# Kernel tuning notes

Hardware: AMD Instinct MI355X
Metric: run time of the kernel (lower is better)

The kernel has to match this reference:

```python
import jax, jax.numpy as jnp
import numpy as np

I, H, FC = 118, 1024, 16

def gru_cell(x, h, Wih, Whh, bih, bhh):
    # torch GRU gate order: r, z, n
    gi = x @ Wih.T + bih          # [B, 3H]
    gh = h @ Whh.T + bhh          # [B, 3H]
    i_r, i_z, i_n = jnp.split(gi, 3, axis=-1)
    h_r, h_z, h_n = jnp.split(gh, 3, axis=-1)
    r = jax.nn.sigmoid(i_r + h_r)
    z = jax.nn.sigmoid(i_z + h_z)
    n = jnp.tanh(i_n + r * h_n)
    return (1.0 - z) * n + z * h

def _param(key, shape, fan):
    bound = 1.0 / np.sqrt(fan)
    return jax.random.uniform(key, shape, jnp.float32, -bound, bound)

def setup_inputs() -> dict:
    key = jax.random.key(0)
    ks = jax.random.split(key, 24)
    B, T = 64, 512
    inp = {"x": jax.random.normal(ks[0], (B, T, I), jnp.float32)}
    # encoder 2-layer GRU
    inp["e_Wih0"] = _param(ks[1], (3 * H, I), H); inp["e_Whh0"] = _param(ks[2], (3 * H, H), H)
    inp["e_bih0"] = _param(ks[3], (3 * H,), H);   inp["e_bhh0"] = _param(ks[4], (3 * H,), H)
    inp["e_Wih1"] = _param(ks[5], (3 * H, H), H); inp["e_Whh1"] = _param(ks[6], (3 * H, H), H)
    inp["e_bih1"] = _param(ks[7], (3 * H,), H);   inp["e_bhh1"] = _param(ks[8], (3 * H,), H)
    # decoder 2-layer GRU
    inp["d_Wih0"] = _param(ks[9], (3 * H, I), H);  inp["d_Whh0"] = _param(ks[10], (3 * H, H), H)
    inp["d_bih0"] = _param(ks[11], (3 * H,), H);   inp["d_bhh0"] = _param(ks[12], (3 * H,), H)
    inp["d_Wih1"] = _param(ks[13], (3 * H, H), H); inp["d_Whh1"] = _param(ks[14], (3 * H, H), H)
    inp["d_bih1"] = _param(ks[15], (3 * H,), H);   inp["d_bhh1"] = _param(ks[16], (3 * H,), H)
    # decoder head
    inp["fc_W"] = _param(ks[17], (FC, H), H);  inp["fc_b"] = _param(ks[18], (FC,), H)
    inp["out_W"] = _param(ks[19], (1, FC), FC); inp["out_b"] = _param(ks[20], (1,), FC)
    return inp

def reference(x, e_Wih0, e_Whh0, e_bih0, e_bhh0, e_Wih1, e_Whh1, e_bih1, e_bhh1,
              d_Wih0, d_Whh0, d_bih0, d_bhh0, d_Wih1, d_Whh1, d_bih1, d_bhh1,
              fc_W, fc_b, out_W, out_b):
    B = x.shape[0]
    h1 = jnp.zeros((B, H), x.dtype)
    h2 = jnp.zeros((B, H), x.dtype)

    def enc_step(carry, xt):
        h1, h2 = carry
        h1 = gru_cell(xt, h1, e_Wih0, e_Whh0, e_bih0, e_bhh0)
        h2 = gru_cell(h1, h2, e_Wih1, e_Whh1, e_bih1, e_bhh1)
        return (h1, h2), None

    (h1, h2), _ = jax.lax.scan(enc_step, (h1, h2), jnp.swapaxes(x, 0, 1))  # scan over T

    # decoder: single step (target_length == 1)
    dec_in = x[:, -1, :]                                  # [B, I]
    h1 = gru_cell(dec_in, h1, d_Wih0, d_Whh0, d_bih0, d_bhh0)
    h2 = gru_cell(h1, h2, d_Wih1, d_Whh1, d_bih1, d_bhh1)
    y = jax.nn.relu(h2 @ fc_W.T + fc_b)                   # [B, FC]
    y = y @ out_W.T + out_b                               # [B, 1]
    return y
```

## Files before the change

kernel.cpp:

```cpp
#include <hip/hip_runtime.h>
#include <hip/hip_bf16.h>

#define H_DIM 1024
#define B_DIM 64
#define T_DIM 512
#define I_PAD 128
#define I_ORIG 118
#define FC_DIM 16
#define HB (B_DIM * H_DIM)

typedef __hip_bfloat16 bf16;
typedef __attribute__((ext_vector_type(8))) short short8v;
typedef __attribute__((ext_vector_type(4))) float f32x4;

#define MFMA16(a, b, c) __builtin_amdgcn_mfma_f32_16x16x32_bf16(a, b, c, 0, 0, 0)

__device__ __forceinline__ short8v ldg8(const bf16* p) {
    return *reinterpret_cast<const short8v*>(p);
}
__device__ __forceinline__ short8v ld_byp16(const bf16* p) {
    union { unsigned long long u[2]; short8v v; } r;
    const unsigned long long* q = reinterpret_cast<const unsigned long long*>(p);
    r.u[0] = __hip_atomic_load(q,     __ATOMIC_RELAXED, __HIP_MEMORY_SCOPE_AGENT);
    r.u[1] = __hip_atomic_load(q + 1, __ATOMIC_RELAXED, __HIP_MEMORY_SCOPE_AGENT);
    return r.v;
}
__device__ __forceinline__ unsigned short f2bf_bits(float f) {
    union { bf16 h; unsigned short s; } u;
    u.h = __float2bfloat16(f);
    return u.s;
}
__device__ __forceinline__ unsigned ld_coh(const unsigned* p) {
    return __hip_atomic_load(p, __ATOMIC_RELAXED, __HIP_MEMORY_SCOPE_AGENT);
}
__device__ __forceinline__ void st_coh(unsigned* p, unsigned v) {
    __hip_atomic_store(p, v, __ATOMIC_RELAXED, __HIP_MEMORY_SCOPE_AGENT);
}

__global__ __launch_bounds__(256) void cvt_x_kernel(
    const float* __restrict__ x, bf16* __restrict__ out)
{
    int idx  = blockIdx.x * 256 + threadIdx.x;
    int c    = idx & 127;
    int rest = idx >> 7;
    int b    = rest & 63;
    int t    = rest >> 6;
    float v  = (c < I_ORIG) ? x[((long)b * T_DIM + t) * I_ORIG + c] : 0.0f;
    out[idx] = __float2bfloat16(v);
}

__global__ __launch_bounds__(256) void cvt_pad(
    const float* __restrict__ in, bf16* __restrict__ out,
    int kin, int kp, long total)
{
    long idx = (long)blockIdx.x * 256 + threadIdx.x;
    if (idx >= total) return;
    int  c = (int)(idx % kp);
    long r = idx / kp;
    out[idx] = __float2bfloat16(c < kin ? in[r * kin + c] : 0.0f);
}

template<int WXK, bool WXG, bool SEQ>
__global__ __launch_bounds__(256, 1) void gru_pass(
    const bf16* __restrict__ xbase, long xstride,
    const bf16* __restrict__ WxG,
    const bf16* __restrict__ WhG,
    const float* __restrict__ bih, const float* __restrict__ bhh,
    const bf16* hin,
    bf16* hout,
    const float* f_init, float* f_final,
    int nsteps, unsigned* flags)
{
    extern __shared__ char smem[];
    constexpr int WH_BYTES = 3 * 16 * 1024 * 2;
    constexpr int WX_BYTES = WXG ? 0 : 3 * 16 * WXK * 2;
    float* sm_red = (float*)(smem + WH_BYTES + WX_BYTES);

    const int tid  = threadIdx.x;
    const int w    = tid >> 6;
    const int lane = tid & 63;
    const int ln   = lane & 15;
    const int lk   = lane >> 4;
    const int bid  = blockIdx.x;
    const int bn   = bid & 63;
    const int grp  = bid >> 6;
    const int j0   = bn * 16;
    const int m0   = grp * 16;
    const int j    = j0 + ln;

    for (int c = tid; c < WH_BYTES / 16; c += 256) {
        int lin = c * 16;
        int row = lin >> 11;
        int wb  = lin & 2047;
        int g   = row >> 4, jj = row & 15;
        const bf16* src = WhG + ((long)(g * 1024 + j0 + jj) << 10) + (wb >> 1);
        *reinterpret_cast<short8v*>(smem + (lin ^ ((jj & 7) << 4))) = ldg8(src);
    }
    if constexpr (!WXG) {
        for (int c = tid; c < WX_BYTES / 16; c += 256) {
            int lin = c * 16;
            int row = lin / (WXK * 2);
            int wb  = lin % (WXK * 2);
            int g   = row >> 4, jj = row & 15;
            const bf16* src = WxG + (long)(g * 1024 + j0 + jj) * WXK + (wb >> 1);
            *reinterpret_cast<short8v*>(smem + WH_BYTES + (lin ^ ((jj & 7) << 4))) = ldg8(src);
        }
    }
    __syncthreads();

    const int wkoh = w << 8;
    const int wkox = (WXK == 128) ? (w << 5) : (w << 8);
    const int swz  = (ln & 7) << 4;
    const int whb0 = ln * 2048 + ((wkoh + lk * 8) << 1);

    const float bias_r  = bih[j] + bhh[j];
    const float bias_z  = bih[j + H_DIM] + bhh[j + H_DIM];
    const float bias_ni = bih[j + 2 * H_DIM];
    const float bias_nh = bhh[j + 2 * H_DIM];

    const int  crow = (w << 2) | lk;
    const int  gm   = m0 + crow;
    const long opos = (long)gm * H_DIM + j;

    float hprev = f_init ? f_init[opos] : 0.0f;

    unsigned* myflag = flags ? flags + (grp << 8) + (bn << 2) + w : nullptr;
    const unsigned* pollp = flags ? flags + (grp << 8) + (w << 6) + lane : nullptr;

    constexpr int NKX = (WXK == 128) ? 1 : 8;
    short8v xcur[NKX];
    {
        const bf16* xr = xbase + (long)(m0 + ln) * WXK + wkox + lk * 8;
#pragma unroll
        for (int ks = 0; ks < NKX; ++ks) xcur[ks] = ldg8(xr + ks * 32);
    }

    for (int t = 0; t < nsteps; ++t) {
        f32x4 aR{0,0,0,0}, aZ{0,0,0,0}, aNI{0,0,0,0}, aNH{0,0,0,0};

        if constexpr (WXK == 128) {
            int o = WH_BYTES + ln * 256 + ((wkox + lk * 8) << 1);
            short8v br  = *(const short8v*)(smem + ((o       ) ^ swz));
            short8v bz  = *(const short8v*)(smem + ((o + 4096) ^ swz));
            short8v bnn = *(const short8v*)(smem + ((o + 8192) ^ swz));
            aR  = MFMA16(xcur[0], br,  aR);
            aZ  = MFMA16(xcur[0], bz,  aZ);
            aNI = MFMA16(xcur[0], bnn, aNI);
        } else {
            const bf16* wxr = WxG + (long)(j0 + ln) * 1024 + wkox + lk * 8;
#pragma unroll
            for (int ks = 0; ks < 8; ++ks) {
                short8v br  = ldg8(wxr + ks * 32);
                short8v bz  = ldg8(wxr + (1 << 20) + ks * 32);
                short8v bnn = ldg8(wxr + (2 << 20) + ks * 32);
                aR  = MFMA16(xcur[ks], br,  aR);
                aZ  = MFMA16(xcur[ks], bz,  aZ);
                aNI = MFMA16(xcur[ks], bnn, aNI);
            }
        }

        if (flags && t > 0) {
            const unsigned tgt = (unsigned)t;
            while (true) {
                unsigned fv = ld_coh(pollp);
                if (__all((int)(fv >= tgt))) break;
            }
            asm volatile("" ::: "memory");
        }

        const bf16* bf_in = SEQ ? hin + (long)t * HB : hin + (long)(t & 1) * HB;
        const bf16* ha = bf_in + (long)(m0 + ln) * H_DIM + wkoh + lk * 8;
        short8v ah[8];
#pragma unroll
        for (int ks = 0; ks < 8; ++ks)
            ah[ks] = SEQ ? ldg8(ha + ks * 32) : ld_byp16(ha + ks * 32);

#pragma unroll
        for (int ks = 0; ks < 8; ++ks) {
            int o = whb0 + ks * 64;
            short8v br  = *(const short8v*)(smem + ((o        ) ^ swz));
            short8v bz  = *(const short8v*)(smem + ((o + 32768) ^ swz));
            short8v bnn = *(const short8v*)(smem + ((o + 65536) ^ swz));
            aR  = MFMA16(ah[ks], br,  aR);
            aZ  = MFMA16(ah[ks], bz,  aZ);
            aNH = MFMA16(ah[ks], bnn, aNH);
        }

        float* red = sm_red + (t & 1) * 4608;
#pragma unroll
        for (int a = 0; a < 4; ++a) {
            f32x4 v = (a == 0) ? aR : (a == 1) ? aZ : (a == 2) ? aNI : aNH;
            int base = ((w << 2) + a) * 288 + (lk * 4) * 18 + ln;
#pragma unroll
            for (int e = 0; e < 4; ++e)
                red[base + e * 18] = v[e];
        }
        __syncthreads();

        float sR = 0, sZ = 0, sNI = 0, sNH = 0;
#pragma unroll
        for (int w2 = 0; w2 < 4; ++w2) {
            int tb = (w2 << 2) * 288 + crow * 18 + ln;
            sR  += red[tb];
            sZ  += red[tb + 288];
            sNI += red[tb + 576];
            sNH += red[tb + 864];
        }
        float rr = 1.0f / (1.0f + __expf(-(sR + bias_r)));
        float zz = 1.0f / (1.0f + __expf(-(sZ + bias_z)));
        float xn = (sNI + bias_ni) + rr * (sNH + bias_nh);
        float nn = 2.0f / (1.0f + __expf(-2.0f * xn)) - 1.0f;
        float hv = (1.0f - zz) * nn + zz * hprev;
        hprev = hv;

        {
            bf16* wr = SEQ ? hout + (long)t * HB
                           : const_cast<bf16*>(hin) + (long)((t + 1) & 1) * HB;
            float ho = __shfl_xor(hv, 1);
            if ((ln & 1) == 0) {
                unsigned pk = (unsigned)f2bf_bits(hv)
                            | ((unsigned)f2bf_bits(ho) << 16);
                st_coh((unsigned*)(wr + (opos & ~1L)), pk);
            }
        }

        if (flags && t + 1 < nsteps) {
            asm volatile("s_waitcnt vmcnt(0)" ::: "memory");
            if (lane == 0) st_coh(myflag, (unsigned)(t + 1));
        }

        if (t + 1 < nsteps) {
            const bf16* xr = xbase + (long)(t + 1) * xstride
                             + (long)(m0 + ln) * WXK + wkox + lk * 8;
#pragma unroll
            for (int ks = 0; ks < NKX; ++ks) xcur[ks] = ldg8(xr + ks * 32);
        }

        if (t == nsteps - 1 && f_final) f_final[opos] = hv;
    }
}

__global__ __launch_bounds__(1024) void head_kernel(
    const float* __restrict__ h2,
    const float* __restrict__ fc_W, const float* __restrict__ fc_b,
    const float* __restrict__ out_W, const float* __restrict__ out_b,
    float* __restrict__ y)
{
    __shared__ float acc_s[FC_DIM][B_DIM];
    const int b = threadIdx.x & 63;
    const int f = threadIdx.x >> 6;
    const float* wp = fc_W + (long)f * H_DIM;
    const float* hp = h2 + (long)b * H_DIM;
    float a = fc_b[f];
#pragma unroll 8
    for (int k = 0; k < H_DIM; ++k)
        a = fmaf(hp[k], wp[k], a);
    a = fmaxf(a, 0.0f);
    acc_s[f][b] = a * out_W[f];
    __syncthreads();
    if (threadIdx.x < 64) {
        float s = out_b[0];
#pragma unroll
        for (int f2 = 0; f2 < FC_DIM; ++f2) s += acc_s[f2][b];
        y[b] = s;
    }
}

extern "C" void kernel_launch(void* const* d_in, const int* in_sizes, int n_in,
                              void* d_out, int out_size, void* d_ws, size_t ws_size,
                              hipStream_t stream)
{
    const float* x      = (const float*)d_in[0];
    const float* e_Wih0 = (const float*)d_in[1];
    const float* e_Whh0 = (const float*)d_in[2];
    const float* e_bih0 = (const float*)d_in[3];
    const float* e_bhh0 = (const float*)d_in[4];
    const float* e_Wih1 = (const float*)d_in[5];
    const float* e_Whh1 = (const float*)d_in[6];
    const float* e_bih1 = (const float*)d_in[7];
    const float* e_bhh1 = (const float*)d_in[8];
    const float* d_Wih0 = (const float*)d_in[9];
    const float* d_Whh0 = (const float*)d_in[10];
    const float* d_bih0 = (const float*)d_in[11];
    const float* d_bhh0 = (const float*)d_in[12];
    const float* d_Wih1 = (const float*)d_in[13];
    const float* d_Whh1 = (const float*)d_in[14];
    const float* d_bih1 = (const float*)d_in[15];
    const float* d_bhh1 = (const float*)d_in[16];
    const float* fc_W   = (const float*)d_in[17];
    const float* fc_b   = (const float*)d_in[18];
    const float* out_W  = (const float*)d_in[19];
    const float* out_b  = (const float*)d_in[20];
    (void)in_sizes; (void)n_in; (void)out_size; (void)ws_size;

    char* p = (char*)d_ws;
    auto alloc = [&](size_t bytes) -> char* {
        char* r = p; p += (bytes + 255) & ~(size_t)255; return r;
    };
    bf16*  x_bf  = (bf16*)alloc((size_t)T_DIM * B_DIM * I_PAD * 2);
    bf16*  wih0e = (bf16*)alloc(3072ull * 128 * 2);
    bf16*  whh0e = (bf16*)alloc(3072ull * 1024 * 2);
    bf16*  wih1e = (bf16*)alloc(3072ull * 1024 * 2);
    bf16*  whh1e = (bf16*)alloc(3072ull * 1024 * 2);
    bf16*  wih0d = (bf16*)alloc(3072ull * 128 * 2);
    bf16*  whh0d = (bf16*)alloc(3072ull * 1024 * 2);
    bf16*  wih1d = (bf16*)alloc(3072ull * 1024 * 2);
    bf16*  whh1d = (bf16*)alloc(3072ull * 1024 * 2);
    bf16*  h1all = (bf16*)alloc(513ull * HB * 2);
    bf16*  h2pp  = (bf16*)alloc(2ull * HB * 2);
    bf16*  hd1b  = (bf16*)alloc((size_t)HB * 2);
    bf16*  hd2b  = (bf16*)alloc((size_t)HB * 2);
    float* hf1f  = (float*)alloc((size_t)HB * 4);
    float* hf2f  = (float*)alloc((size_t)HB * 4);
    float* hd1f  = (float*)alloc((size_t)HB * 4);
    float* hd2f  = (float*)alloc((size_t)HB * 4);
    unsigned* fl1 = (unsigned*)alloc(4096);
    unsigned* fl2 = (unsigned*)alloc(4096);

    constexpr int RED = 2 * 4608 * 4;
    constexpr int S1  = 98304 + 12288 + RED;
    constexpr int S2  = 98304 + RED;
    (void)hipFuncSetAttribute((const void*)gru_pass<128, false, true>,
                              hipFuncAttributeMaxDynamicSharedMemorySize, S1);
    (void)hipFuncSetAttribute((const void*)gru_pass<1024, true, false>,
                              hipFuncAttributeMaxDynamicSharedMemorySize, S2);
    (void)hipFuncSetAttribute((const void*)gru_pass<1024, true, true>,
                              hipFuncAttributeMaxDynamicSharedMemorySize, S2);

    cvt_x_kernel<<<(T_DIM * B_DIM * I_PAD) / 256, 256, 0, stream>>>(x, x_bf);
    auto cvt = [&](const float* in, bf16* out, int kin, int kp) {
        long total = 3072L * kp;
        cvt_pad<<<(int)((total + 255) / 256), 256, 0, stream>>>(in, out, kin, kp, total);
    };
    cvt(e_Wih0, wih0e, 118, 128);
    cvt(e_Whh0, whh0e, 1024, 1024);
    cvt(e_Wih1, wih1e, 1024, 1024);
    cvt(e_Whh1, whh1e, 1024, 1024);
    cvt(d_Wih0, wih0d, 118, 128);
    cvt(d_Whh0, whh0d, 1024, 1024);
    cvt(d_Wih1, wih1d, 1024, 1024);
    cvt(d_Whh1, whh1d, 1024, 1024);

    hipMemsetAsync(h1all, 0, (size_t)HB * 2, stream);
    hipMemsetAsync(h2pp,  0, 2ull * HB * 2, stream);
    hipMemsetAsync(fl1,   0, 4096, stream);
    hipMemsetAsync(fl2,   0, 4096, stream);

    gru_pass<128, false, true><<<256, 256, S1, stream>>>(
        x_bf, (long)B_DIM * I_PAD, wih0e, whh0e, e_bih0, e_bhh0,
        h1all, h1all + HB, nullptr, hf1f, T_DIM, fl1);

    gru_pass<1024, true, false><<<256, 256, S2, stream>>>(
        h1all + HB, (long)HB, wih1e, whh1e, e_bih1, e_bhh1,
        h2pp, nullptr, nullptr, hf2f, T_DIM, fl2);

    gru_pass<128, false, true><<<256, 256, S1, stream>>>(
        x_bf + 511L * B_DIM * I_PAD, 0, wih0d, whh0d, d_bih0, d_bhh0,
        h1all + 512L * HB, hd1b, hf1f, hd1f, 1, nullptr);

    gru_pass<1024, true, true><<<256, 256, S2, stream>>>(
        hd1b, 0, wih1d, whh1d, d_bih1, d_bhh1,
        h2pp, hd2b, hf2f, hd2f, 1, nullptr);

    head_kernel<<<1, 1024, 0, stream>>>(hd2f, fc_W, fc_b, out_W, out_b,
                                        (float*)d_out);
}
```

Baseline: 4.154 ms.

## Fuse both encoder GRU layers into one persistent wavefront-pipelined kernel

Replaces the two sequential encoder layer launches with one persistent kernel. Blocks 0-127 run layer 1 and blocks 128-255 run layer 2, with layer 2 trailing one timestep behind through shared per-step flags polled as 64-bit words. Each block now covers 32 batch rows with a K-split across wave pairs, reduced through double-buffered shared memory, and biases are folded into the accumulators. This overlaps the two layers' recurrences instead of running them back to back, but each layer gets half the blocks, so per-step work per block doubles and cross-layer flag polling adds latency. The decoder passes are rewired to the new buffers, and the now-unused flag and prefetch logic is removed from gru_pass.

```diff
diff --git a/kernel.cpp b/kernel.cpp
--- a/kernel.cpp
+++ b/kernel.cpp
@@ -30,11 +30,11 @@
     u.h = __float2bfloat16(f);
     return u.s;
 }
-__device__ __forceinline__ unsigned ld_coh(const unsigned* p) {
-    return __hip_atomic_load(p, __ATOMIC_RELAXED, __HIP_MEMORY_SCOPE_AGENT);
-}
 __device__ __forceinline__ void st_coh(unsigned* p, unsigned v) {
     __hip_atomic_store(p, v, __ATOMIC_RELAXED, __HIP_MEMORY_SCOPE_AGENT);
+}
+__device__ __forceinline__ unsigned long long ld_coh64(const unsigned long long* p) {
+    return __hip_atomic_load(p, __ATOMIC_RELAXED, __HIP_MEMORY_SCOPE_AGENT);
 }
 
 __global__ __launch_bounds__(256) void cvt_x_kernel(
@@ -60,14 +60,277 @@
     out[idx] = __float2bfloat16(c < kin ? in[r * kin + c] : 0.0f);
 }
 
+__global__ __launch_bounds__(256, 1) void gru_fused(
+    const bf16* __restrict__ x_bf,
+    const bf16* __restrict__ Wx1, const bf16* __restrict__ Wh1,
+    const bf16* __restrict__ Wx2, const bf16* __restrict__ Wh2,
+    const float* __restrict__ bih1, const float* __restrict__ bhh1,
+    const float* __restrict__ bih2, const float* __restrict__ bhh2,
+    bf16* h1all, bf16* h2pp,
+    float* hf1f, float* hf2f,
+    unsigned* flags)
+{
+    extern __shared__ char smem[];
+    constexpr int WH = 98304;
+    constexpr int WX = 12288;
+    constexpr int REDF = 4352;
+    float* redbase = (float*)(smem + WH + WX);
+
+    const int tid  = threadIdx.x;
+    const int w    = tid >> 6;
+    const int lane = tid & 63;
+    const int ln   = lane & 15;
+    const int lk   = lane >> 4;
+    const int bid  = blockIdx.x;
+    const int lyr  = bid >> 7;
+    const int mh   = (bid >> 6) & 1;
+    const int bn   = bid & 63;
+    const int ms   = w >> 1;
+    const int kh   = w & 1;
+    const int j0   = bn << 4;
+    const int m0   = mh << 5;
+    const int j    = j0 + ln;
+
+    const bf16* WhG = lyr ? Wh2 : Wh1;
+    for (int c = tid; c < WH / 16; c += 256) {
+        int lin = c * 16;
+        int row = lin >> 11;
+        int wb  = lin & 2047;
+        int g   = row >> 4, jj = row & 15;
+        const bf16* src = WhG + ((long)(g * 1024 + j0 + jj) << 10) + (wb >> 1);
+        *reinterpret_cast<short8v*>(smem + (lin ^ ((jj & 7) << 4))) = ldg8(src);
+    }
+    if (lyr == 0) {
+        for (int c = tid; c < WX / 16; c += 256) {
+            int lin = c * 16;
+            int row = lin >> 8;
+            int wb  = lin & 255;
+            int g   = row >> 4, jj = row & 15;
+            const bf16* src = Wx1 + (long)(g * 1024 + j0 + jj) * I_PAD + (wb >> 1);
+            *reinterpret_cast<short8v*>(smem + WH + (lin ^ ((jj & 7) << 4))) = ldg8(src);
+        }
+    }
+    __syncthreads();
+
+    const float* bihv = lyr ? bih2 : bih1;
+    const float* bhhv = lyr ? bhh2 : bhh1;
+    const float kb   = (kh == 0) ? 1.0f : 0.0f;
+    const float b_r  = (bihv[j] + bhhv[j]) * kb;
+    const float b_z  = (bihv[j + 1024] + bhhv[j + 1024]) * kb;
+    const float b_ni = bihv[j + 2048] * kb;
+    const float b_nh = bhhv[j + 2048] * kb;
+
+    const int swz  = (ln & 7) << 4;
+    const int whb0 = ln * 2048 + kh * 1024 + lk * 16;
+    const int wxb0 = WH + ln * 256 + kh * 128 + lk * 16;
+    const long arow = m0 + (ms << 4) + ln;
+    const int  rl0  = (w << 3) + lk;
+    const int  tgrp = ((ms << 1) | kh) << 2;
+
+    const unsigned long long* pollp =
+        (const unsigned long long*)flags +
+        ((mh << 8) | (((kh << 5) | (lane & 31)) << 2) | ((ms << 1) | (lane >> 5)));
+    unsigned* myflag = flags + ((((mh << 8) | (bn << 2) | w) << 1) | lyr);
+
+    float hp0 = 0.0f, hp1 = 0.0f;
+
+    if (lyr == 0) {
+        short8v xc0, xc1;
+        {
+            const bf16* xr = x_bf + arow * I_PAD + kh * 64 + lk * 8;
+            xc0 = ldg8(xr); xc1 = ldg8(xr + 32);
+        }
+        for (int t = 0; t < T_DIM; ++t) {
+            f32x4 aR0{b_r,b_r,b_r,b_r}, aZ0{b_z,b_z,b_z,b_z};
+            f32x4 aNI{b_ni,b_ni,b_ni,b_ni}, aNH0{b_nh,b_nh,b_nh,b_nh};
+            f32x4 aR1{0,0,0,0}, aZ1{0,0,0,0}, aNH1{0,0,0,0};
+
+            {
+                int o = wxb0;
+                short8v br  = *(const short8v*)(smem + ((o       ) ^ swz));
+                short8v bz  = *(const short8v*)(smem + ((o + 4096) ^ swz));
+                short8v bnn = *(const short8v*)(smem + ((o + 8192) ^ swz));
+                aR0 = MFMA16(xc0, br, aR0); aZ0 = MFMA16(xc0, bz, aZ0);
+                aNI = MFMA16(xc0, bnn, aNI);
+                o = wxb0 + 64;
+                br  = *(const short8v*)(smem + ((o       ) ^ swz));
+                bz  = *(const short8v*)(smem + ((o + 4096) ^ swz));
+                bnn = *(const short8v*)(smem + ((o + 8192) ^ swz));
+                aR1 = MFMA16(xc1, br, aR1); aZ1 = MFMA16(xc1, bz, aZ1);
+                aNI = MFMA16(xc1, bnn, aNI);
+            }
+
+            {
+                const unsigned tgt = (unsigned)t;
+                while (true) {
+                    unsigned long long fv = ld_coh64(pollp);
+                    if (__all((int)((unsigned)fv >= tgt))) break;
+                }
+                asm volatile("" ::: "memory");
+            }
+
+            const bf16* ha = h1all + (long)t * HB + arow * H_DIM + kh * 512 + lk * 8;
+            short8v ah[16];
+#pragma unroll
+            for (int ks = 0; ks < 16; ++ks) ah[ks] = ldg8(ha + ks * 32);
+#pragma unroll
+            for (int ks = 0; ks < 16; ++ks) {
+                int o = whb0 + ks * 64;
+                short8v br  = *(const short8v*)(smem + ((o        ) ^ swz));
+                short8v bz  = *(const short8v*)(smem + ((o + 32768) ^ swz));
+                short8v bnn = *(const short8v*)(smem + ((o + 65536) ^ swz));
+                if (ks & 1) { aR1 = MFMA16(ah[ks], br, aR1); aZ1 = MFMA16(ah[ks], bz, aZ1); aNH1 = MFMA16(ah[ks], bnn, aNH1); }
+                else        { aR0 = MFMA16(ah[ks], br, aR0); aZ0 = MFMA16(ah[ks], bz, aZ0); aNH0 = MFMA16(ah[ks], bnn, aNH0); }
+            }
+            f32x4 vR = aR0 + aR1, vZ = aZ0 + aZ1, vNH = aNH0 + aNH1, vNI = aNI;
+
+            float* red = redbase + (t & 1) * REDF;
+#pragma unroll
+            for (int a = 0; a < 4; ++a) {
+                f32x4 v = (a == 0) ? vR : (a == 1) ? vZ : (a == 2) ? vNI : vNH;
+                int base = (tgrp + a) * 272 + (lk << 2) * 17 + ln;
+#pragma unroll
+                for (int e = 0; e < 4; ++e) red[base + e * 17] = v[e];
+            }
+            __syncthreads();
+
+            float hv0, hv1;
+#pragma unroll
+            for (int e2 = 0; e2 < 2; ++e2) {
+                int rl = rl0 + (e2 << 2);
+                int msrc = rl >> 4, rr = rl & 15;
+                int b0 = (msrc << 3) * 272 + rr * 17 + ln;
+                int b1 = b0 + 4 * 272;
+                float sR  = red[b0] + red[b1];
+                float sZ  = red[b0 + 272] + red[b1 + 272];
+                float sNI = red[b0 + 544] + red[b1 + 544];
+                float sNH = red[b0 + 816] + red[b1 + 816];
+                float rr_ = 1.0f / (1.0f + __expf(-sR));
+                float zz  = 1.0f / (1.0f + __expf(-sZ));
+                float xn  = sNI + rr_ * sNH;
+                float nn  = 2.0f / (1.0f + __expf(-2.0f * xn)) - 1.0f;
+                float hp  = e2 ? hp1 : hp0;
+                float hv  = (1.0f - zz) * nn + zz * hp;
+                if (e2) { hp1 = hv; hv1 = hv; } else { hp0 = hv; hv0 = hv; }
+            }
+            bf16* outslot = h1all + (long)(t + 1) * HB;
+            float ho0 = __shfl_xor(hv0, 1), ho1 = __shfl_xor(hv1, 1);
+            if ((ln & 1) == 0) {
+                unsigned p0 = (unsigned)f2bf_bits(hv0) | ((unsigned)f2bf_bits(ho0) << 16);
+                unsigned p1 = (unsigned)f2bf_bits(hv1) | ((unsigned)f2bf_bits(ho1) << 16);
+                st_coh((unsigned*)(outslot + (long)(m0 + rl0) * 1024 + (j & ~1)), p0);
+                st_coh((unsigned*)(outslot + (long)(m0 + rl0 + 4) * 1024 + (j & ~1)), p1);
+            }
+            if (t == T_DIM - 1) {
+                hf1f[(long)(m0 + rl0) * 1024 + j] = hv0;
+                hf1f[(long)(m0 + rl0 + 4) * 1024 + j] = hv1;
+            }
+            asm volatile("s_waitcnt vmcnt(0)" ::: "memory");
+            if (lane == 0) st_coh(myflag, (unsigned)(t + 1));
+            if (t + 1 < T_DIM) {
+                const bf16* xr = x_bf + (long)(t + 1) * (B_DIM * I_PAD)
+                               + arow * I_PAD + kh * 64 + lk * 8;
+                xc0 = ldg8(xr); xc1 = ldg8(xr + 32);
+            }
+        }
+    } else {
+        const bf16* wxr = Wx2 + (long)j * 1024 + kh * 512 + lk * 8;
+        for (int t = 0; t < T_DIM; ++t) {
+            {
+                const unsigned t1 = (unsigned)(t + 1), t0 = (unsigned)t;
+                while (true) {
+                    unsigned long long fv = ld_coh64(pollp);
+                    unsigned f1 = (unsigned)fv, f2 = (unsigned)(fv >> 32);
+                    if (__all((int)((f1 >= t1) & (f2 >= t0)))) break;
+                }
+                asm volatile("" ::: "memory");
+            }
+
+            const bf16* xa = h1all + (long)(t + 1) * HB + arow * H_DIM + kh * 512 + lk * 8;
+            const bf16* ha = h2pp + (long)(t & 1) * HB + arow * H_DIM + kh * 512 + lk * 8;
+            short8v ai[16], ah[16];
+#pragma unroll
+            for (int ks = 0; ks < 16; ++ks) ai[ks] = ldg8(xa + ks * 32);
+#pragma unroll
+            for (int ks = 0; ks < 16; ++ks) ah[ks] = ld_byp16(ha + ks * 32);
+
+            f32x4 aR0{b_r,b_r,b_r,b_r}, aZ0{b_z,b_z,b_z,b_z};
+            f32x4 aNI0{b_ni,b_ni,b_ni,b_ni}, aNH0{b_nh,b_nh,b_nh,b_nh};
+            f32x4 aR1{0,0,0,0}, aZ1{0,0,0,0}, aNI1{0,0,0,0}, aNH1{0,0,0,0};
+
+#pragma unroll
+            for (int ks = 0; ks < 16; ++ks) {
+                short8v br  = ldg8(wxr + ks * 32);
+                short8v bz  = ldg8(wxr + (1 << 20) + ks * 32);
+                short8v bnn = ldg8(wxr + (2 << 20) + ks * 32);
+                if (ks & 1) { aR1 = MFMA16(ai[ks], br, aR1); aZ1 = MFMA16(ai[ks], bz, aZ1); aNI1 = MFMA16(ai[ks], bnn, aNI1); }
+                else        { aR0 = MFMA16(ai[ks], br, aR0); aZ0 = MFMA16(ai[ks], bz, aZ0); aNI0 = MFMA16(ai[ks], bnn, aNI0); }
+            }
+#pragma unroll
+            for (int ks = 0; ks < 16; ++ks) {
+                int o = whb0 + ks * 64;
+                short8v br  = *(const short8v*)(smem + ((o        ) ^ swz));
+                short8v bz  = *(const short8v*)(smem + ((o + 32768) ^ swz));
+                short8v bnn = *(const short8v*)(smem + ((o + 65536) ^ swz));
+                if (ks & 1) { aR1 = MFMA16(ah[ks], br, aR1); aZ1 = MFMA16(ah[ks], bz, aZ1); aNH1 = MFMA16(ah[ks], bnn, aNH1); }
+                else        { aR0 = MFMA16(ah[ks], br, aR0); aZ0 = MFMA16(ah[ks], bz, aZ0); aNH0 = MFMA16(ah[ks], bnn, aNH0); }
+            }
+            f32x4 vR = aR0 + aR1, vZ = aZ0 + aZ1, vNI = aNI0 + aNI1, vNH = aNH0 + aNH1;
+
+            float* red = redbase + (t & 1) * REDF;
+#pragma unroll
+            for (int a = 0; a < 4; ++a) {
+                f32x4 v = (a == 0) ? vR : (a == 1) ? vZ : (a == 2) ? vNI : vNH;
+                int base = (tgrp + a) * 272 + (lk << 2) * 17 + ln;
+#pragma unroll
+                for (int e = 0; e < 4; ++e) red[base + e * 17] = v[e];
+            }
+            __syncthreads();
+
+            float hv0, hv1;
+#pragma unroll
+            for (int e2 = 0; e2 < 2; ++e2) {
+                int rl = rl0 + (e2 << 2);
+                int msrc = rl >> 4, rr = rl & 15;
+                int b0 = (msrc << 3) * 272 + rr * 17 + ln;
+                int b1 = b0 + 4 * 272;
+                float sR  = red[b0] + red[b1];
+                float sZ  = red[b0 + 272] + red[b1 + 272];
+                float sNI = red[b0 + 544] + red[b1 + 544];
+                float sNH = red[b0 + 816] + red[b1 + 816];
+                float rr_ = 1.0f / (1.0f + __expf(-sR));
+                float zz  = 1.0f / (1.0f + __expf(-sZ));
+                float xn  = sNI + rr_ * sNH;
+                float nn  = 2.0f / (1.0f + __expf(-2.0f * xn)) - 1.0f;
+                float hp  = e2 ? hp1 : hp0;
+                float hv  = (1.0f - zz) * nn + zz * hp;
+                if (e2) { hp1 = hv; hv1 = hv; } else { hp0 = hv; hv0 = hv; }
+            }
+            bf16* outslot = h2pp + (long)((t + 1) & 1) * HB;
+            float ho0 = __shfl_xor(hv0, 1), ho1 = __shfl_xor(hv1, 1);
+            if ((ln & 1) == 0) {
+                unsigned p0 = (unsigned)f2bf_bits(hv0) | ((unsigned)f2bf_bits(ho0) << 16);
+                unsigned p1 = (unsigned)f2bf_bits(hv1) | ((unsigned)f2bf_bits(ho1) << 16);
+                st_coh((unsigned*)(outslot + (long)(m0 + rl0) * 1024 + (j & ~1)), p0);
+                st_coh((unsigned*)(outslot + (long)(m0 + rl0 + 4) * 1024 + (j & ~1)), p1);
+            }
+            if (t == T_DIM - 1) {
+                hf2f[(long)(m0 + rl0) * 1024 + j] = hv0;
+                hf2f[(long)(m0 + rl0 + 4) * 1024 + j] = hv1;
+            }
+            asm volatile("s_waitcnt vmcnt(0)" ::: "memory");
+            if (lane == 0) st_coh(myflag, (unsigned)(t + 1));
+        }
+    }
+}
+
 template<int WXK, bool WXG, bool SEQ>
 __global__ __launch_bounds__(256, 1) void gru_pass(
     const bf16* __restrict__ xbase, long xstride,
     const bf16* __restrict__ WxG,
     const bf16* __restrict__ WhG,
     const float* __restrict__ bih, const float* __restrict__ bhh,
-    const bf16* hin,
-    bf16* hout,
+    const bf16* hin, bf16* hout,
     const float* f_init, float* f_final,
     int nsteps, unsigned* flags)
 {
@@ -124,9 +387,6 @@
 
     float hprev = f_init ? f_init[opos] : 0.0f;
 
-    unsigned* myflag = flags ? flags + (grp << 8) + (bn << 2) + w : nullptr;
-    const unsigned* pollp = flags ? flags + (grp << 8) + (w << 6) + lane : nullptr;
-
     constexpr int NKX = (WXK == 128) ? 1 : 8;
     short8v xcur[NKX];
     {
@@ -159,15 +419,6 @@
             }
         }
 
-        if (flags && t > 0) {
-            const unsigned tgt = (unsigned)t;
-            while (true) {
-                unsigned fv = ld_coh(pollp);
-                if (__all((int)(fv >= tgt))) break;
-            }
-            asm volatile("" ::: "memory");
-        }
-
         const bf16* bf_in = SEQ ? hin + (long)t * HB : hin + (long)(t & 1) * HB;
         const bf16* ha = bf_in + (long)(m0 + ln) * H_DIM + wkoh + lk * 8;
         short8v ah[8];
@@ -223,20 +474,8 @@
                 st_coh((unsigned*)(wr + (opos & ~1L)), pk);
             }
         }
-
-        if (flags && t + 1 < nsteps) {
-            asm volatile("s_waitcnt vmcnt(0)" ::: "memory");
-            if (lane == 0) st_coh(myflag, (unsigned)(t + 1));
-        }
-
-        if (t + 1 < nsteps) {
-            const bf16* xr = xbase + (long)(t + 1) * xstride
-                             + (long)(m0 + ln) * WXK + wkox + lk * 8;
-#pragma unroll
-            for (int ks = 0; ks < NKX; ++ks) xcur[ks] = ldg8(xr + ks * 32);
-        }
-
         if (t == nsteps - 1 && f_final) f_final[opos] = hv;
+        (void)flags;
     }
 }
 
@@ -306,25 +545,23 @@
     bf16*  whh0d = (bf16*)alloc(3072ull * 1024 * 2);
     bf16*  wih1d = (bf16*)alloc(3072ull * 1024 * 2);
     bf16*  whh1d = (bf16*)alloc(3072ull * 1024 * 2);
-    bf16*  h1all = (bf16*)alloc(513ull * HB * 2);
+    bf16*  h1all = (bf16*)alloc(514ull * HB * 2);
     bf16*  h2pp  = (bf16*)alloc(2ull * HB * 2);
-    bf16*  hd1b  = (bf16*)alloc((size_t)HB * 2);
-    bf16*  hd2b  = (bf16*)alloc((size_t)HB * 2);
     float* hf1f  = (float*)alloc((size_t)HB * 4);
     float* hf2f  = (float*)alloc((size_t)HB * 4);
     float* hd1f  = (float*)alloc((size_t)HB * 4);
     float* hd2f  = (float*)alloc((size_t)HB * 4);
-    unsigned* fl1 = (unsigned*)alloc(4096);
-    unsigned* fl2 = (unsigned*)alloc(4096);
-
+    unsigned* fl = (unsigned*)alloc(4096);
+
+    constexpr int SF = 98304 + 12288 + 2 * 17408;
     constexpr int RED = 2 * 4608 * 4;
     constexpr int S1  = 98304 + 12288 + RED;
     constexpr int S2  = 98304 + RED;
-    (void)hipFuncSetAttribute((const void*)gru_pass<128, false, true>,
+    (void)hipFuncSetAttribute((const void*)gru_fused,
+                              hipFuncAttributeMaxDynamicSharedMemorySize, SF);
+    (void)hipFuncSetAttribute((const void*)gru_pass<128, false, false>,
                               hipFuncAttributeMaxDynamicSharedMemorySize, S1);
     (void)hipFuncSetAttribute((const void*)gru_pass<1024, true, false>,
-                              hipFuncAttributeMaxDynamicSharedMemorySize, S2);
-    (void)hipFuncSetAttribute((const void*)gru_pass<1024, true, true>,
                               hipFuncAttributeMaxDynamicSharedMemorySize, S2);
 
     cvt_x_kernel<<<(T_DIM * B_DIM * I_PAD) / 256, 256, 0, stream>>>(x, x_bf);
@@ -343,24 +580,20 @@
 
     hipMemsetAsync(h1all, 0, (size_t)HB * 2, stream);
     hipMemsetAsync(h2pp,  0, 2ull * HB * 2, stream);
-    hipMemsetAsync(fl1,   0, 4096, stream);
-    hipMemsetAsync(fl2,   0, 4096, stream);
-
-    gru_pass<128, false, true><<<256, 256, S1, stream>>>(
-        x_bf, (long)B_DIM * I_PAD, wih0e, whh0e, e_bih0, e_bhh0,
-        h1all, h1all + HB, nullptr, hf1f, T_DIM, fl1);
+    hipMemsetAsync(fl,    0, 4096, stream);
+
+    gru_fused<<<256, 256, SF, stream>>>(
+        x_bf, wih0e, whh0e, wih1e, whh1e,
+        e_bih0, e_bhh0, e_bih1, e_bhh1,
+        h1all, h2pp, hf1f, hf2f, fl);
+
+    gru_pass<128, false, false><<<256, 256, S1, stream>>>(
+        x_bf + 511L * B_DIM * I_PAD, 0, wih0d, whh0d, d_bih0, d_bhh0,
+        h1all + 512L * HB, nullptr, hf1f, hd1f, 1, nullptr);
 
     gru_pass<1024, true, false><<<256, 256, S2, stream>>>(
-        h1all + HB, (long)HB, wih1e, whh1e, e_bih1, e_bhh1,
-        h2pp, nullptr, nullptr, hf2f, T_DIM, fl2);
-
-    gru_pass<128, false, true><<<256, 256, S1, stream>>>(
-        x_bf + 511L * B_DIM * I_PAD, 0, wih0d, whh0d, d_bih0, d_bhh0,
-        h1all + 512L * HB, hd1b, hf1f, hd1f, 1, nullptr);
-
-    gru_pass<1024, true, true><<<256, 256, S2, stream>>>(
-        hd1b, 0, wih1d, whh1d, d_bih1, d_bhh1,
-        h2pp, hd2b, hf2f, hd2f, 1, nullptr);
+        h1all + 513L * HB, 0, wih1d, whh1d, d_bih1, d_bhh1,
+        h2pp, nullptr, hf2f, hd2f, 1, nullptr);
 
     head_kernel<<<1, 1024, 0, stream>>>(hd2f, fc_W, fc_b, out_W, out_b,
                                         (float*)d_out);
```

Measured after the change: 8.074 ms. +94.4%, slower.

## Fuse both encoder GRU layers into one wavefront-pipelined persistent kernel

Applied to the files above, without the earlier changes.

Replaces the two back-to-back encoder layer launches with a single persistent kernel. Each round, every block advances layer 1 at step r and layer 2 at step r-2, so both layers share one flag-based grid barrier per round instead of running 512 serial steps each. Layer-2 hidden state now lives in a 4-slot ring, and the h1 fragments from the previous round are reused as layer-2 input. The cost is a heavier per-round body, since layer 2 still streams its weights from global memory, and two extra pipeline fill/drain rounds.

```diff
diff --git a/kernel.cpp b/kernel.cpp
--- a/kernel.cpp
+++ b/kernel.cpp
@@ -60,21 +60,24 @@
     out[idx] = __float2bfloat16(c < kin ? in[r * kin + c] : 0.0f);
 }
 
-template<int WXK, bool WXG, bool SEQ>
-__global__ __launch_bounds__(256, 1) void gru_pass(
-    const bf16* __restrict__ xbase, long xstride,
-    const bf16* __restrict__ WxG,
-    const bf16* __restrict__ WhG,
-    const float* __restrict__ bih, const float* __restrict__ bhh,
-    const bf16* hin,
-    bf16* hout,
-    const float* f_init, float* f_final,
-    int nsteps, unsigned* flags)
+__global__ __launch_bounds__(256, 1) void gru_mega(
+    const bf16* __restrict__ x_bf,
+    const bf16* __restrict__ Wx1,
+    const bf16* __restrict__ Wh1,
+    const bf16* __restrict__ Wx2,
+    const bf16* __restrict__ Wh2,
+    const float* __restrict__ bih1, const float* __restrict__ bhh1,
+    const float* __restrict__ bih2, const float* __restrict__ bhh2,
+    bf16* h1all,
+    bf16* h2ring,
+    float* hf1f, float* hf2f,
+    unsigned* flags)
 {
     extern __shared__ char smem[];
-    constexpr int WH_BYTES = 3 * 16 * 1024 * 2;
-    constexpr int WX_BYTES = WXG ? 0 : 3 * 16 * WXK * 2;
-    float* sm_red = (float*)(smem + WH_BYTES + WX_BYTES);
+    constexpr int WH = 3 * 16 * 1024 * 2;
+    constexpr int WX = 3 * 16 * 128 * 2;
+    float* red1 = (float*)(smem + WH + WX);
+    float* red2 = red1 + 4608;
 
     const int tid  = threadIdx.x;
     const int w    = tid >> 6;
@@ -88,6 +91,248 @@
     const int m0   = grp * 16;
     const int j    = j0 + ln;
 
+    for (int c = tid; c < WH / 16; c += 256) {
+        int lin = c * 16;
+        int row = lin >> 11;
+        int wb  = lin & 2047;
+        int g   = row >> 4, jj = row & 15;
+        const bf16* src = Wh1 + ((long)(g * 1024 + j0 + jj) << 10) + (wb >> 1);
+        *reinterpret_cast<short8v*>(smem + (lin ^ ((jj & 7) << 4))) = ldg8(src);
+    }
+    for (int c = tid; c < WX / 16; c += 256) {
+        int lin = c * 16;
+        int row = lin >> 8;
+        int wb  = lin & 255;
+        int g   = row >> 4, jj = row & 15;
+        const bf16* src = Wx1 + (long)(g * 1024 + j0 + jj) * I_PAD + (wb >> 1);
+        *reinterpret_cast<short8v*>(smem + WH + (lin ^ ((jj & 7) << 4))) = ldg8(src);
+    }
+    __syncthreads();
+
+    const int wko  = w << 8;
+    const int wkox = w << 5;
+    const int swz  = (ln & 7) << 4;
+    const int whb0 = ln * 2048 + ((wko + lk * 8) << 1);
+
+    const float b1r  = bih1[j] + bhh1[j];
+    const float b1z  = bih1[j + 1024] + bhh1[j + 1024];
+    const float b1ni = bih1[j + 2048];
+    const float b1nh = bhh1[j + 2048];
+    const float b2r  = bih2[j] + bhh2[j];
+    const float b2z  = bih2[j + 1024] + bhh2[j + 1024];
+    const float b2ni = bih2[j + 2048];
+    const float b2nh = bhh2[j + 2048];
+
+    const int  crow = (w << 2) | lk;
+    const int  gm   = m0 + crow;
+    const long opos = (long)gm * H_DIM + j;
+
+    const bf16* wx2r = Wx2 + (long)j * 1024 + wko + lk * 8;
+    const bf16* wh2r = Wh2 + (long)j * 1024 + wko + lk * 8;
+
+    unsigned* myflag = flags + (grp << 8) + (bn << 2) + w;
+    const unsigned* pollp = flags + (grp << 8) + (w << 6) + lane;
+
+    float hprev1 = 0.0f, hprev2 = 0.0f;
+    short8v ah1p[8];
+    short8v xcur;
+    {
+        const bf16* xr = x_bf + (long)(m0 + ln) * I_PAD + wkox + lk * 8;
+        xcur = ldg8(xr);
+    }
+
+    const int NR = T_DIM + 2;
+    for (int r = 0; r < NR; ++r) {
+        const bool doL1  = (r < T_DIM);
+        const bool doL2  = (r >= 2);
+        const bool doLd1 = (r <= T_DIM);
+
+        f32x4 aR{0,0,0,0}, aZ{0,0,0,0}, aNI{0,0,0,0}, aNH{0,0,0,0};
+        f32x4 cR{0,0,0,0}, cZ{0,0,0,0}, cNI{0,0,0,0}, cNH{0,0,0,0};
+
+        if (doL1) {
+            int o = WH + ln * 256 + ((wkox + lk * 8) << 1);
+            short8v br  = *(const short8v*)(smem + ((o       ) ^ swz));
+            short8v bz  = *(const short8v*)(smem + ((o + 4096) ^ swz));
+            short8v bnn = *(const short8v*)(smem + ((o + 8192) ^ swz));
+            aR  = MFMA16(xcur, br,  aR);
+            aZ  = MFMA16(xcur, bz,  aZ);
+            aNI = MFMA16(xcur, bnn, aNI);
+        }
+        if (doL2) {
+#pragma unroll
+            for (int ks = 0; ks < 8; ++ks) {
+                short8v br  = ldg8(wx2r + ks * 32);
+                short8v bz  = ldg8(wx2r + (1 << 20) + ks * 32);
+                short8v bnn = ldg8(wx2r + (2 << 20) + ks * 32);
+                cR  = MFMA16(ah1p[ks], br,  cR);
+                cZ  = MFMA16(ah1p[ks], bz,  cZ);
+                cNI = MFMA16(ah1p[ks], bnn, cNI);
+            }
+        }
+
+        if (r > 0) {
+            const unsigned tgt = (unsigned)r;
+            while (true) {
+                unsigned fv = ld_coh(pollp);
+                if (__all((int)(fv >= tgt))) break;
+            }
+            asm volatile("" ::: "memory");
+        }
+
+        short8v ah1[8], ah2[8];
+        if (doLd1) {
+            const bf16* ha = h1all + (long)r * HB + (long)(m0 + ln) * H_DIM
+                             + wko + lk * 8;
+#pragma unroll
+            for (int ks = 0; ks < 8; ++ks) ah1[ks] = ldg8(ha + ks * 32);
+        }
+        if (doL2) {
+            const bf16* hb = h2ring + (long)((r - 1) & 3) * HB
+                             + (long)(m0 + ln) * H_DIM + wko + lk * 8;
+#pragma unroll
+            for (int ks = 0; ks < 8; ++ks) ah2[ks] = ld_byp16(hb + ks * 32);
+        }
+
+        if (doL1) {
+#pragma unroll
+            for (int ks = 0; ks < 8; ++ks) {
+                int o = whb0 + ks * 64;
+                short8v br  = *(const short8v*)(smem + ((o        ) ^ swz));
+                short8v bz  = *(const short8v*)(smem + ((o + 32768) ^ swz));
+                short8v bnn = *(const short8v*)(smem + ((o + 65536) ^ swz));
+                aR  = MFMA16(ah1[ks], br,  aR);
+                aZ  = MFMA16(ah1[ks], bz,  aZ);
+                aNH = MFMA16(ah1[ks], bnn, aNH);
+            }
+        }
+        if (doL2) {
+#pragma unroll
+            for (int ks = 0; ks < 8; ++ks) {
+                short8v br  = ldg8(wh2r + ks * 32);
+                short8v bz  = ldg8(wh2r + (1 << 20) + ks * 32);
+                short8v bnn = ldg8(wh2r + (2 << 20) + ks * 32);
+                cR  = MFMA16(ah2[ks], br,  cR);
+                cZ  = MFMA16(ah2[ks], bz,  cZ);
+                cNH = MFMA16(ah2[ks], bnn, cNH);
+            }
+        }
+
+        __syncthreads();
+        if (doL1) {
+#pragma unroll
+            for (int a = 0; a < 4; ++a) {
+                f32x4 v = (a == 0) ? aR : (a == 1) ? aZ : (a == 2) ? aNI : aNH;
+                int base = ((w << 2) + a) * 288 + (lk * 4) * 18 + ln;
+#pragma unroll
+                for (int e = 0; e < 4; ++e) red1[base + e * 18] = v[e];
+            }
+        }
+        if (doL2) {
+#pragma unroll
+            for (int a = 0; a < 4; ++a) {
+                f32x4 v = (a == 0) ? cR : (a == 1) ? cZ : (a == 2) ? cNI : cNH;
+                int base = ((w << 2) + a) * 288 + (lk * 4) * 18 + ln;
+#pragma unroll
+                for (int e = 0; e < 4; ++e) red2[base + e * 18] = v[e];
+            }
+        }
+        __syncthreads();
+
+        if (doL1) {
+            float sR = 0, sZ = 0, sNI = 0, sNH = 0;
+#pragma unroll
+            for (int w2 = 0; w2 < 4; ++w2) {
+                int tb = (w2 << 2) * 288 + crow * 18 + ln;
+                sR  += red1[tb];
+                sZ  += red1[tb + 288];
+                sNI += red1[tb + 576];
+                sNH += red1[tb + 864];
+            }
+            float rr = 1.0f / (1.0f + __expf(-(sR + b1r)));
+            float zz = 1.0f / (1.0f + __expf(-(sZ + b1z)));
+            float xn = (sNI + b1ni) + rr * (sNH + b1nh);
+            float nn = 2.0f / (1.0f + __expf(-2.0f * xn)) - 1.0f;
+            float hv = (1.0f - zz) * nn + zz * hprev1;
+            hprev1 = hv;
+            bf16* dst = h1all + (long)(r + 1) * HB;
+            float ho = __shfl_xor(hv, 1);
+            if ((ln & 1) == 0) {
+                unsigned pk = (unsigned)f2bf_bits(hv)
+                            | ((unsigned)f2bf_bits(ho) << 16);
+                st_coh((unsigned*)(dst + (opos & ~1L)), pk);
+            }
+            if (r == T_DIM - 1) hf1f[opos] = hv;
+        }
+        if (doL2) {
+            float sR = 0, sZ = 0, sNI = 0, sNH = 0;
+#pragma unroll
+            for (int w2 = 0; w2 < 4; ++w2) {
+                int tb = (w2 << 2) * 288 + crow * 18 + ln;
+                sR  += red2[tb];
+                sZ  += red2[tb + 288];
+                sNI += red2[tb + 576];
+                sNH += red2[tb + 864];
+            }
+            float rr = 1.0f / (1.0f + __expf(-(sR + b2r)));
+            float zz = 1.0f / (1.0f + __expf(-(sZ + b2z)));
+            float xn = (sNI + b2ni) + rr * (sNH + b2nh);
+            float nn = 2.0f / (1.0f + __expf(-2.0f * xn)) - 1.0f;
+            float hv = (1.0f - zz) * nn + zz * hprev2;
+            hprev2 = hv;
+            bf16* dst = h2ring + (long)(r & 3) * HB;
+            float ho = __shfl_xor(hv, 1);
+            if ((ln & 1) == 0) {
+                unsigned pk = (unsigned)f2bf_bits(hv)
+                            | ((unsigned)f2bf_bits(ho) << 16);
+                st_coh((unsigned*)(dst + (opos & ~1L)), pk);
+            }
+            if (r == NR - 1) hf2f[opos] = hv;
+        }
+
+        if (r + 1 < NR) {
+            asm volatile("s_waitcnt vmcnt(0)" ::: "memory");
+            if (lane == 0) st_coh(myflag, (unsigned)(r + 1));
+        }
+        if (r + 1 < T_DIM) {
+            const bf16* xr = x_bf + (long)(r + 1) * (B_DIM * I_PAD)
+                             + (long)(m0 + ln) * I_PAD + wkox + lk * 8;
+            xcur = ldg8(xr);
+        }
+        if (doLd1) {
+#pragma unroll
+            for (int ks = 0; ks < 8; ++ks) ah1p[ks] = ah1[ks];
+        }
+    }
+}
+
+template<int WXK, bool WXG, bool SEQ>
+__global__ __launch_bounds__(256, 1) void gru_pass(
+    const bf16* __restrict__ xbase, long xstride,
+    const bf16* __restrict__ WxG,
+    const bf16* __restrict__ WhG,
+    const float* __restrict__ bih, const float* __restrict__ bhh,
+    const bf16* hin, bf16* hout,
+    const float* f_init, float* f_final,
+    int nsteps, unsigned* flags)
+{
+    extern __shared__ char smem[];
+    constexpr int WH_BYTES = 3 * 16 * 1024 * 2;
+    constexpr int WX_BYTES = WXG ? 0 : 3 * 16 * WXK * 2;
+    float* sm_red = (float*)(smem + WH_BYTES + WX_BYTES);
+
+    const int tid  = threadIdx.x;
+    const int w    = tid >> 6;
+    const int lane = tid & 63;
+    const int ln   = lane & 15;
+    const int lk   = lane >> 4;
+    const int bid  = blockIdx.x;
+    const int bn   = bid & 63;
+    const int grp  = bid >> 6;
+    const int j0   = bn * 16;
+    const int m0   = grp * 16;
+    const int j    = j0 + ln;
+
     for (int c = tid; c < WH_BYTES / 16; c += 256) {
         int lin = c * 16;
         int row = lin >> 11;
@@ -123,9 +368,6 @@
     const long opos = (long)gm * H_DIM + j;
 
     float hprev = f_init ? f_init[opos] : 0.0f;
-
-    unsigned* myflag = flags ? flags + (grp << 8) + (bn << 2) + w : nullptr;
-    const unsigned* pollp = flags ? flags + (grp << 8) + (w << 6) + lane : nullptr;
 
     constexpr int NKX = (WXK == 128) ? 1 : 8;
     short8v xcur[NKX];
@@ -159,15 +401,6 @@
             }
         }
 
-        if (flags && t > 0) {
-            const unsigned tgt = (unsigned)t;
-            while (true) {
-                unsigned fv = ld_coh(pollp);
-                if (__all((int)(fv >= tgt))) break;
-            }
-            asm volatile("" ::: "memory");
-        }
-
         const bf16* bf_in = SEQ ? hin + (long)t * HB : hin + (long)(t & 1) * HB;
         const bf16* ha = bf_in + (long)(m0 + ln) * H_DIM + wkoh + lk * 8;
         short8v ah[8];
@@ -223,20 +456,8 @@
                 st_coh((unsigned*)(wr + (opos & ~1L)), pk);
             }
         }
-
-        if (flags && t + 1 < nsteps) {
-            asm volatile("s_waitcnt vmcnt(0)" ::: "memory");
-            if (lane == 0) st_coh(myflag, (unsigned)(t + 1));
-        }
-
-        if (t + 1 < nsteps) {
-            const bf16* xr = xbase + (long)(t + 1) * xstride
-                             + (long)(m0 + ln) * WXK + wkox + lk * 8;
-#pragma unroll
-            for (int ks = 0; ks < NKX; ++ks) xcur[ks] = ldg8(xr + ks * 32);
-        }
-
         if (t == nsteps - 1 && f_final) f_final[opos] = hv;
+        (void)flags;
     }
 }
 
@@ -306,25 +527,25 @@
     bf16*  whh0d = (bf16*)alloc(3072ull * 1024 * 2);
     bf16*  wih1d = (bf16*)alloc(3072ull * 1024 * 2);
     bf16*  whh1d = (bf16*)alloc(3072ull * 1024 * 2);
-    bf16*  h1all = (bf16*)alloc(513ull * HB * 2);
-    bf16*  h2pp  = (bf16*)alloc(2ull * HB * 2);
+    bf16*  h1all = (bf16*)alloc(514ull * HB * 2);
+    bf16*  h2rg  = (bf16*)alloc(4ull * HB * 2);
     bf16*  hd1b  = (bf16*)alloc((size_t)HB * 2);
     bf16*  hd2b  = (bf16*)alloc((size_t)HB * 2);
     float* hf1f  = (float*)alloc((size_t)HB * 4);
     float* hf2f  = (float*)alloc((size_t)HB * 4);
     float* hd1f  = (float*)alloc((size_t)HB * 4);
     float* hd2f  = (float*)alloc((size_t)HB * 4);
-    unsigned* fl1 = (unsigned*)alloc(4096);
-    unsigned* fl2 = (unsigned*)alloc(4096);
+    unsigned* fl = (unsigned*)alloc(4096);
 
     constexpr int RED = 2 * 4608 * 4;
+    constexpr int SM  = 98304 + 12288 + RED;
     constexpr int S1  = 98304 + 12288 + RED;
     constexpr int S2  = 98304 + RED;
+    (void)hipFuncSetAttribute((const void*)gru_mega,
+                              hipFuncAttributeMaxDynamicSharedMemorySize, SM);
     (void)hipFuncSetAttribute((const void*)gru_pass<128, false, true>,
                               hipFuncAttributeMaxDynamicSharedMemorySize, S1);
     (void)hipFuncSetAttribute((const void*)gru_pass<1024, true, false>,
-                              hipFuncAttributeMaxDynamicSharedMemorySize, S2);
-    (void)hipFuncSetAttribute((const void*)gru_pass<1024, true, true>,
                               hipFuncAttributeMaxDynamicSharedMemorySize, S2);
 
     cvt_x_kernel<<<(T_DIM * B_DIM * I_PAD) / 256, 256, 0, stream>>>(x, x_bf);
@@ -342,25 +563,21 @@
     cvt(d_Whh1, whh1d, 1024, 1024);
 
     hipMemsetAsync(h1all, 0, (size_t)HB * 2, stream);
-    hipMemsetAsync(h2pp,  0, 2ull * HB * 2, stream);
-    hipMemsetAsync(fl1,   0, 4096, stream);
-    hipMemsetAsync(fl2,   0, 4096, stream);
-
-    gru_pass<128, false, true><<<256, 256, S1, stream>>>(
-        x_bf, (long)B_DIM * I_PAD, wih0e, whh0e, e_bih0, e_bhh0,
-        h1all, h1all + HB, nullptr, hf1f, T_DIM, fl1);
-
-    gru_pass<1024, true, false><<<256, 256, S2, stream>>>(
-        h1all + HB, (long)HB, wih1e, whh1e, e_bih1, e_bhh1,
-        h2pp, nullptr, nullptr, hf2f, T_DIM, fl2);
+    hipMemsetAsync(h2rg,  0, 2ull * HB * 2, stream);
+    hipMemsetAsync(fl,    0, 4096, stream);
+
+    gru_mega<<<256, 256, SM, stream>>>(
+        x_bf, wih0e, whh0e, wih1e, whh1e,
+        e_bih0, e_bhh0, e_bih1, e_bhh1,
+        h1all, h2rg, hf1f, hf2f, fl);
 
     gru_pass<128, false, true><<<256, 256, S1, stream>>>(
         x_bf + 511L * B_DIM * I_PAD, 0, wih0d, whh0d, d_bih0, d_bhh0,
         h1all + 512L * HB, hd1b, hf1f, hd1f, 1, nullptr);
 
-    gru_pass<1024, true, true><<<256, 256, S2, stream>>>(
+    gru_pass<1024, true, false><<<256, 256, S2, stream>>>(
         hd1b, 0, wih1d, whh1d, d_bih1, d_bhh1,
-        h2pp, hd2b, hf2f, hd2f, 1, nullptr);
+        h2rg + 1L * HB, hd2b, hf2f, hd2f, 1, nullptr);
 
     head_kernel<<<1, 1024, 0, stream>>>(hd2f, fc_W, fc_b, out_W, out_b,
                                         (float*)d_out);
```

Measured after the change: 5.387 ms. +29.7%, slower.

## Keep recurrent GRU weight fragments in registers instead of LDS

Applied to the files above, without the earlier changes.

Each block now loads its slice of the recurrent weight matrix (and the small input weight for layer 0) straight into per-thread register arrays once, replacing the swizzled shared-memory staging and the per-step LDS reads. The dynamic shared memory is reduced to a static reduction buffer. This removes LDS read traffic from every step of the 512-step serial loop. The cost is 24 extra 16-byte register vectors per thread, which raises register pressure and could cause spills.

```diff
diff --git a/kernel.cpp b/kernel.cpp
--- a/kernel.cpp
+++ b/kernel.cpp
@@ -60,21 +60,18 @@
     out[idx] = __float2bfloat16(c < kin ? in[r * kin + c] : 0.0f);
 }
 
-template<int WXK, bool WXG, bool SEQ>
+template<int WXK, bool SEQ>
 __global__ __launch_bounds__(256, 1) void gru_pass(
     const bf16* __restrict__ xbase, long xstride,
-    const bf16* __restrict__ WxG,
-    const bf16* __restrict__ WhG,
+    const bf16* __restrict__ Wx,
+    const bf16* __restrict__ Wh,
     const float* __restrict__ bih, const float* __restrict__ bhh,
     const bf16* hin,
     bf16* hout,
     const float* f_init, float* f_final,
     int nsteps, unsigned* flags)
 {
-    extern __shared__ char smem[];
-    constexpr int WH_BYTES = 3 * 16 * 1024 * 2;
-    constexpr int WX_BYTES = WXG ? 0 : 3 * 16 * WXK * 2;
-    float* sm_red = (float*)(smem + WH_BYTES + WX_BYTES);
+    __shared__ float sm_red[2 * 4608];
 
     const int tid  = threadIdx.x;
     const int w    = tid >> 6;
@@ -88,40 +85,35 @@
     const int m0   = grp * 16;
     const int j    = j0 + ln;
 
-    for (int c = tid; c < WH_BYTES / 16; c += 256) {
-        int lin = c * 16;
-        int row = lin >> 11;
-        int wb  = lin & 2047;
-        int g   = row >> 4, jj = row & 15;
-        const bf16* src = WhG + ((long)(g * 1024 + j0 + jj) << 10) + (wb >> 1);
-        *reinterpret_cast<short8v*>(smem + (lin ^ ((jj & 7) << 4))) = ldg8(src);
-    }
-    if constexpr (!WXG) {
-        for (int c = tid; c < WX_BYTES / 16; c += 256) {
-            int lin = c * 16;
-            int row = lin / (WXK * 2);
-            int wb  = lin % (WXK * 2);
-            int g   = row >> 4, jj = row & 15;
-            const bf16* src = WxG + (long)(g * 1024 + j0 + jj) * WXK + (wb >> 1);
-            *reinterpret_cast<short8v*>(smem + WH_BYTES + (lin ^ ((jj & 7) << 4))) = ldg8(src);
-        }
-    }
-    __syncthreads();
-
     const int wkoh = w << 8;
     const int wkox = (WXK == 128) ? (w << 5) : (w << 8);
-    const int swz  = (ln & 7) << 4;
-    const int whb0 = ln * 2048 + ((wkoh + lk * 8) << 1);
+    const int crow = (w << 2) | lk;
+    const int gm   = m0 + crow;
+    const long opos = (long)gm * H_DIM + j;
+
+    short8v whr[8], whz[8], whn[8];
+    {
+        const bf16* bp = Wh + (long)j * 1024 + wkoh + lk * 8;
+#pragma unroll
+        for (int ks = 0; ks < 8; ++ks) {
+            whr[ks] = ldg8(bp + ks * 32);
+            whz[ks] = ldg8(bp + (1 << 20) + ks * 32);
+            whn[ks] = ldg8(bp + (2 << 20) + ks * 32);
+        }
+    }
+    short8v wx_r{}, wx_z{}, wx_n{};
+    if constexpr (WXK == 128) {
+        const bf16* bx = Wx + (long)j * I_PAD + wkox + lk * 8;
+        wx_r = ldg8(bx);
+        wx_z = ldg8(bx + (1 << 17));
+        wx_n = ldg8(bx + (2 << 17));
+    }
 
     const float bias_r  = bih[j] + bhh[j];
     const float bias_z  = bih[j + H_DIM] + bhh[j + H_DIM];
     const float bias_ni = bih[j + 2 * H_DIM];
     const float bias_nh = bhh[j + 2 * H_DIM];
 
-    const int  crow = (w << 2) | lk;
-    const int  gm   = m0 + crow;
-    const long opos = (long)gm * H_DIM + j;
-
     float hprev = f_init ? f_init[opos] : 0.0f;
 
     unsigned* myflag = flags ? flags + (grp << 8) + (bn << 2) + w : nullptr;
@@ -139,15 +131,11 @@
         f32x4 aR{0,0,0,0}, aZ{0,0,0,0}, aNI{0,0,0,0}, aNH{0,0,0,0};
 
         if constexpr (WXK == 128) {
-            int o = WH_BYTES + ln * 256 + ((wkox + lk * 8) << 1);
-            short8v br  = *(const short8v*)(smem + ((o       ) ^ swz));
-            short8v bz  = *(const short8v*)(smem + ((o + 4096) ^ swz));
-            short8v bnn = *(const short8v*)(smem + ((o + 8192) ^ swz));
-            aR  = MFMA16(xcur[0], br,  aR);
-            aZ  = MFMA16(xcur[0], bz,  aZ);
-            aNI = MFMA16(xcur[0], bnn, aNI);
+            aR  = MFMA16(xcur[0], wx_r, aR);
+            aZ  = MFMA16(xcur[0], wx_z, aZ);
+            aNI = MFMA16(xcur[0], wx_n, aNI);
         } else {
-            const bf16* wxr = WxG + (long)(j0 + ln) * 1024 + wkox + lk * 8;
+            const bf16* wxr = Wx + (long)j * 1024 + wkox + lk * 8;
 #pragma unroll
             for (int ks = 0; ks < 8; ++ks) {
                 short8v br  = ldg8(wxr + ks * 32);
@@ -174,16 +162,11 @@
 #pragma unroll
         for (int ks = 0; ks < 8; ++ks)
             ah[ks] = SEQ ? ldg8(ha + ks * 32) : ld_byp16(ha + ks * 32);
-
 #pragma unroll
         for (int ks = 0; ks < 8; ++ks) {
-            int o = whb0 + ks * 64;
-            short8v br  = *(const short8v*)(smem + ((o        ) ^ swz));
-            short8v bz  = *(const short8v*)(smem + ((o + 32768) ^ swz));
-            short8v bnn = *(const short8v*)(smem + ((o + 65536) ^ swz));
-            aR  = MFMA16(ah[ks], br,  aR);
-            aZ  = MFMA16(ah[ks], bz,  aZ);
-            aNH = MFMA16(ah[ks], bnn, aNH);
+            aR  = MFMA16(ah[ks], whr[ks], aR);
+            aZ  = MFMA16(ah[ks], whz[ks], aZ);
+            aNH = MFMA16(ah[ks], whn[ks], aNH);
         }
 
         float* red = sm_red + (t & 1) * 4608;
@@ -228,7 +211,6 @@
             asm volatile("s_waitcnt vmcnt(0)" ::: "memory");
             if (lane == 0) st_coh(myflag, (unsigned)(t + 1));
         }
-
         if (t + 1 < nsteps) {
             const bf16* xr = xbase + (long)(t + 1) * xstride
                              + (long)(m0 + ln) * WXK + wkox + lk * 8;
@@ -317,16 +299,6 @@
     unsigned* fl1 = (unsigned*)alloc(4096);
     unsigned* fl2 = (unsigned*)alloc(4096);
 
-    constexpr int RED = 2 * 4608 * 4;
-    constexpr int S1  = 98304 + 12288 + RED;
-    constexpr int S2  = 98304 + RED;
-    (void)hipFuncSetAttribute((const void*)gru_pass<128, false, true>,
-                              hipFuncAttributeMaxDynamicSharedMemorySize, S1);
-    (void)hipFuncSetAttribute((const void*)gru_pass<1024, true, false>,
-                              hipFuncAttributeMaxDynamicSharedMemorySize, S2);
-    (void)hipFuncSetAttribute((const void*)gru_pass<1024, true, true>,
-                              hipFuncAttributeMaxDynamicSharedMemorySize, S2);
-
     cvt_x_kernel<<<(T_DIM * B_DIM * I_PAD) / 256, 256, 0, stream>>>(x, x_bf);
     auto cvt = [&](const float* in, bf16* out, int kin, int kp) {
         long total = 3072L * kp;
@@ -346,19 +318,19 @@
     hipMemsetAsync(fl1,   0, 4096, stream);
     hipMemsetAsync(fl2,   0, 4096, stream);
 
-    gru_pass<128, false, true><<<256, 256, S1, stream>>>(
+    gru_pass<128, true><<<256, 256, 0, stream>>>(
         x_bf, (long)B_DIM * I_PAD, wih0e, whh0e, e_bih0, e_bhh0,
         h1all, h1all + HB, nullptr, hf1f, T_DIM, fl1);
 
-    gru_pass<1024, true, false><<<256, 256, S2, stream>>>(
+    gru_pass<1024, false><<<256, 256, 0, stream>>>(
         h1all + HB, (long)HB, wih1e, whh1e, e_bih1, e_bhh1,
         h2pp, nullptr, nullptr, hf2f, T_DIM, fl2);
 
-    gru_pass<128, false, true><<<256, 256, S1, stream>>>(
+    gru_pass<128, true><<<256, 256, 0, stream>>>(
         x_bf + 511L * B_DIM * I_PAD, 0, wih0d, whh0d, d_bih0, d_bhh0,
         h1all + 512L * HB, hd1b, hf1f, hd1f, 1, nullptr);
 
-    gru_pass<1024, true, true><<<256, 256, S2, stream>>>(
+    gru_pass<1024, true><<<256, 256, 0, stream>>>(
         hd1b, 0, wih1d, whh1d, d_bih1, d_bhh1,
         h2pp, hd2b, hf2f, hd2f, 1, nullptr);
 
```

Result: no change. 4.184 ms (+0.7%).
